# Kernel tuning notes

Hardware: AMD Instinct MI355X
Metric: run time of the kernel (lower is better)

The kernel has to match this reference:

```python
import jax, jax.numpy as jnp
import numpy as np

V, E, H, B, S, C = 50000, 300, 512, 128, 80, 6
HH = 2 * H  # hidden_dim * num_directions (BiDi=True)


def _gru_dir(x, w_ih, w_hh, b_ih, b_hh, reverse):
    # x: (b, t, e) -> (b, t, h); torch nn.GRU cell math
    Bv, T, _ = x.shape
    Hd = w_hh.shape[1]
    xg = jnp.einsum('bte,ge->btg', x, w_ih) + b_ih  # (b, t, 3h)
    if reverse:
        xg = xg[:, ::-1]
    def step(h, xt):
        gi_r, gi_z, gi_n = jnp.split(xt, 3, axis=-1)
        gh_r, gh_z, gh_n = jnp.split(h @ w_hh.T + b_hh, 3, axis=-1)
        r = jax.nn.sigmoid(gi_r + gh_r)
        z = jax.nn.sigmoid(gi_z + gh_z)
        n = jnp.tanh(gi_n + r * gh_n)
        hn = (1.0 - z) * n + z * h
        return hn, hn
    h0 = jnp.zeros((Bv, Hd), x.dtype)
    _, hs = jax.lax.scan(step, h0, jnp.swapaxes(xg, 0, 1))
    hs = jnp.swapaxes(hs, 0, 1)
    if reverse:
        hs = hs[:, ::-1]
    return hs


def _bigru(x, pf, pb):
    return jnp.concatenate([_gru_dir(x, *pf, reverse=False), _gru_dir(x, *pb, reverse=True)], axis=-1)


def _conv1d(x, w, b, d):
    y = jax.lax.conv_general_dilated(x, w, (1,), 'VALID', rhs_dilation=(d,),
                                     dimension_numbers=('NCH', 'OIH', 'NCH'))
    return y + b[None, :, None]


def _bn(x, g, b, m, v):
    # eval-mode BatchNorm1d with running stats
    return (x - m[None, :, None]) * (g[None, :, None] / jnp.sqrt(v[None, :, None] + 1e-5)) + b[None, :, None]


def setup_inputs():
    key = jax.random.key(0)
    ks = iter(jax.random.split(key, 64))
    def W(*shape):
        return jax.random.normal(next(ks), shape, jnp.float32) * 0.02
    inp = {
        'input_batch': jax.random.randint(next(ks), (B, S), 1, V),
        'choices_batch': jax.random.randint(next(ks), (B, 4, C), 1, V),
        'emb_table': W(V, E),
    }
    for p in ('sg', 'cg'):
        for d in ('f', 'b'):
            inp[p + '_wih_' + d] = W(3 * H, E)
            inp[p + '_whh_' + d] = W(3 * H, H)
            inp[p + '_bih_' + d] = W(3 * H)
            inp[p + '_bhh_' + d] = W(3 * H)
    inp['lin_w'] = W(HH, HH * C)
    inp['lin_b'] = W(HH)
    inp['attn_w'] = W(HH, HH)
    inp['attn_b'] = W(HH)
    inp['c11_w'] = W(HH, S, 3);  inp['c11_b'] = W(HH)
    inp['c13_w'] = W(HH, HH, 3); inp['c13_b'] = W(HH)
    inp['c21_w'] = W(HH, HH, 3); inp['c21_b'] = W(HH)
    inp['c23_w'] = W(HH, HH, 3); inp['c23_b'] = W(HH)
    for i in ('1', '2'):
        inp['bn' + i + '_g'] = jnp.ones((HH,), jnp.float32)
        inp['bn' + i + '_b'] = jnp.zeros((HH,), jnp.float32)
        inp['bn' + i + '_m'] = jnp.zeros((HH,), jnp.float32)
        inp['bn' + i + '_v'] = jnp.ones((HH,), jnp.float32)
    inp['gate_wp'] = W(2 * HH, HH)
    inp['gate_wc'] = W(2 * HH, 2 * HH)
    inp['gate_b'] = W(2 * HH)
    inp['out_wp'] = W(2 * HH, HH)
    inp['out_b'] = W(2 * HH)
    return inp


def reference(input_batch, choices_batch, emb_table,
              sg_wih_f, sg_whh_f, sg_bih_f, sg_bhh_f, sg_wih_b, sg_whh_b, sg_bih_b, sg_bhh_b,
              cg_wih_f, cg_whh_f, cg_bih_f, cg_bhh_f, cg_wih_b, cg_whh_b, cg_bih_b, cg_bhh_b,
              lin_w, lin_b, attn_w, attn_b,
              c11_w, c11_b, c13_w, c13_b, c21_w, c21_b, c23_w, c23_b,
              bn1_g, bn1_b, bn1_m, bn1_v, bn2_g, bn2_b, bn2_m, bn2_v,
              gate_wp, gate_wc, gate_b, out_wp, out_b):
    # --- encode passage: embedding + BiGRU (dropout is eval-mode identity) ---
    sent = _bigru(emb_table[input_batch],
                  (sg_wih_f, sg_whh_f, sg_bih_f, sg_bhh_f),
                  (sg_wih_b, sg_whh_b, sg_bih_b, sg_bhh_b))  # (B, S, 2h)
    cgf = (cg_wih_f, cg_whh_f, cg_bih_f, cg_bhh_f)
    cgb = (cg_wih_b, cg_whh_b, cg_bih_b, cg_bhh_b)

    def choice_vec(tok):  # (B, C) -> (B, 2h)
        g = _bigru(emb_table[tok], cgf, cgb)               # (B, C, 2h)
        return g.reshape(g.shape[0], -1) @ lin_w.T + lin_b

    cvs = [choice_vec(choices_batch[:, i]) for i in range(4)]

    # --- AttnReader: shared Wh/bh, per-choice softmax attention over seq ---
    Wh = jnp.einsum('bsh,hg->bsg', sent, attn_w)  # (B, S, 2h)
    bh = sent @ attn_b                            # (B, S)

    def attn_read(cv):
        a = jax.nn.softmax(jnp.einsum('bsg,bg->bs', Wh, cv) + bh, axis=1)
        return jnp.einsum('bs,bsh->bh', a, sent)  # (B, 2h)

    pars = [attn_read(cv) for cv in cvs]

    # --- IDCNN: Conv1d treats seq dim S as channels (faithful to source) ---
    x = jax.nn.relu(_bn(_conv1d(sent, c11_w, c11_b, 1), bn1_g, bn1_b, bn1_m, bn1_v))
    x = _conv1d(x, c13_w, c13_b, 3)
    x = jax.nn.relu(_bn(_conv1d(x, c21_w, c21_b, 1), bn2_g, bn2_b, bn2_m, bn2_v))
    x = _conv1d(x, c23_w, c23_b, 3)
    P = jnp.max(x, axis=2)  # AdaptiveMaxPool1d(1) + squeeze -> (B, 2h)

    Cs = [jnp.concatenate([cv, par], axis=1) for cv, par in zip(cvs, pars)]  # (B, 4h)

    # --- PointerNet (note: source bug makes out1..out4 all equal C1WP+bC1) ---
    WP = P @ gate_wp.T          # (B, 4h)
    WP_out = P @ out_wp.T       # (B, 4h)
    Cd1 = Cs[0] * jax.nn.sigmoid(WP + Cs[0] @ gate_wc.T + gate_b)
    o1 = jnp.sum(Cd1 * WP_out, axis=1, keepdims=True) + (Cd1 @ out_b)[:, None]  # (B, 1)
    return jnp.concatenate([o1, o1, o1, o1], axis=1)  # (B, 4)
```

## Files before the change

### kernel.cpp

```cpp
#include <hip/hip_runtime.h>

typedef unsigned int u32;
typedef unsigned short u16;
typedef __attribute__((ext_vector_type(4))) float f32x4;
typedef __attribute__((ext_vector_type(8))) short bf16x8;

#define DEV static __device__ __forceinline__

DEV float sigf(float x){ return 1.0f/(1.0f + expf(-x)); }

DEV u16 f2bf(float x){
  u32 u = __float_as_uint(x);
  u32 r = (u + 0x7FFFu + ((u >> 16) & 1u)) >> 16;
  return (u16)r;
}

DEV u32 encf(float f){
  u32 u = __float_as_uint(f);
  return (u & 0x80000000u) ? ~u : (u | 0x80000000u);
}
DEV float decf(u32 e){
  return (e & 0x80000000u) ? __uint_as_float(e ^ 0x80000000u) : __uint_as_float(~e);
}

DEV void gload16(const void* g, void* l){
  __builtin_amdgcn_global_load_lds((const __attribute__((address_space(1))) u32*)g,
                                   (__attribute__((address_space(3))) u32*)l, 16, 0, 0);
}

__global__ __launch_bounds__(256,2) void gemm_bf16(
    const u16* __restrict__ A, const u16* __restrict__ A2,
    const u16* __restrict__ B,
    const float* __restrict__ bias, const float* __restrict__ bias2,
    float* __restrict__ C, float* __restrict__ C2, int ldc,
    int Kp, int ksteps)
{
  __shared__ u16 lds[(128 + 128)*32];
  char* ldsc = (char*)&lds[0];
  const int Boff = 128*64;
  const int tid = threadIdx.x;
  const int l = tid & 63, w = tid >> 6;
  const int n0 = blockIdx.x * 128, m0 = blockIdx.y * 128;
  const u16* Ause = blockIdx.z ? A2 : A;
  const float* buse = blockIdx.z ? bias2 : bias;
  float* Cuse = blockIdx.z ? C2 : C;
  const int wr = w >> 1, wc = w & 1;
  const int lr = l & 15, g = l >> 4;

  f32x4 acc[4][4];
  #pragma unroll
  for (int i=0;i<4;++i)
    #pragma unroll
    for (int j=0;j<4;++j) acc[i][j] = f32x4{0.f,0.f,0.f,0.f};

  for (int ks = 0; ks < ksteps; ++ks) {
    const int i0 = ks*32;
    __syncthreads();
    #pragma unroll
    for (int r = 0; r < 2; ++r) {
      const int rr = w*2 + r;
      const int c = rr*64 + l;
      const int row = c >> 2, bpos = c & 3;
      const int ib = bpos ^ (row & 3);
      gload16(Ause + ((size_t)(m0 + row)*Kp + (i0 + ib*8)), ldsc + rr*1024);
      gload16(B    + ((size_t)(n0 + row)*Kp + (i0 + ib*8)), ldsc + Boff + rr*1024);
    }
    __syncthreads();
    bf16x8 af[4], bfr[4];
    #pragma unroll
    for (int m=0;m<4;++m){
      int o = wr*64 + m*16 + lr;
      af[m] = *(const bf16x8*)(ldsc + o*64 + ((g ^ (o&3))<<4));
    }
    #pragma unroll
    for (int n=0;n<4;++n){
      int pr = wc*64 + n*16 + lr;
      bfr[n] = *(const bf16x8*)(ldsc + Boff + pr*64 + ((g ^ (pr&3))<<4));
    }
    #pragma unroll
    for (int m=0;m<4;++m)
      #pragma unroll
      for (int n=0;n<4;++n)
        acc[m][n] = __builtin_amdgcn_mfma_f32_16x16x32_bf16(af[m], bfr[n], acc[m][n], 0,0,0);
  }

  #pragma unroll
  for (int m=0;m<4;++m){
    int mm = m0 + wr*64 + m*16 + g*4;
    f32x4 bv = *(const f32x4*)(buse + mm);
    #pragma unroll
    for (int n=0;n<4;++n){
      int p = n0 + wc*64 + n*16 + lr;
      f32x4 v;
      #pragma unroll
      for (int r2=0;r2<4;++r2) v[r2] = acc[m][n][r2] + bv[r2];
      *(f32x4*)(Cuse + (size_t)p*ldc + mm) = v;
    }
  }
}

__global__ __launch_bounds__(256,2) void gemm_bf16_sk(
    const u16* __restrict__ A, const u16* __restrict__ B,
    float* __restrict__ C, int ldc, int Kp, int kpc)
{
  __shared__ u16 lds[(128 + 128)*32];
  char* ldsc = (char*)&lds[0];
  const int Boff = 128*64;
  const int tid = threadIdx.x;
  const int l = tid & 63, w = tid >> 6;
  const int n0 = blockIdx.x * 128, m0 = blockIdx.y * 128;
  const int ks0 = blockIdx.z * kpc;
  const int wr = w >> 1, wc = w & 1;
  const int lr = l & 15, g = l >> 4;

  f32x4 acc[4][4];
  #pragma unroll
  for (int i=0;i<4;++i)
    #pragma unroll
    for (int j=0;j<4;++j) acc[i][j] = f32x4{0.f,0.f,0.f,0.f};

  for (int ks = 0; ks < kpc; ++ks) {
    const int i0 = (ks0 + ks)*32;
    __syncthreads();
    #pragma unroll
    for (int r = 0; r < 2; ++r) {
      const int rr = w*2 + r;
      const int c = rr*64 + l;
      const int row = c >> 2, bpos = c & 3;
      const int ib = bpos ^ (row & 3);
      gload16(A + ((size_t)(m0 + row)*Kp + (i0 + ib*8)), ldsc + rr*1024);
      gload16(B + ((size_t)(n0 + row)*Kp + (i0 + ib*8)), ldsc + Boff + rr*1024);
    }
    __syncthreads();
    bf16x8 af[4], bfr[4];
    #pragma unroll
    for (int m=0;m<4;++m){
      int o = wr*64 + m*16 + lr;
      af[m] = *(const bf16x8*)(ldsc + o*64 + ((g ^ (o&3))<<4));
    }
    #pragma unroll
    for (int n=0;n<4;++n){
      int pr = wc*64 + n*16 + lr;
      bfr[n] = *(const bf16x8*)(ldsc + Boff + pr*64 + ((g ^ (pr&3))<<4));
    }
    #pragma unroll
    for (int m=0;m<4;++m)
      #pragma unroll
      for (int n=0;n<4;++n)
        acc[m][n] = __builtin_amdgcn_mfma_f32_16x16x32_bf16(af[m], bfr[n], acc[m][n], 0,0,0);
  }

  #pragma unroll
  for (int m=0;m<4;++m){
    int mm = m0 + wr*64 + m*16 + g*4;
    #pragma unroll
    for (int n=0;n<4;++n){
      int p = n0 + wc*64 + n*16 + lr;
      float* dst = C + (size_t)p*ldc + mm;
      #pragma unroll
      for (int r2=0;r2<4;++r2) atomicAdd(dst + r2, acc[m][n][r2]);
    }
  }
}

__global__ void initc(float* __restrict__ C, const float* __restrict__ bias,
                      int total, int mmask)
{
  int i = blockIdx.x*256 + threadIdx.x;
  if (i < total) C[i] = bias ? bias[i & mmask] : 0.f;
}

__global__ __launch_bounds__(256) void gru_step(
    const float* __restrict__ xg0, const float* __restrict__ xg1,
    const float* __restrict__ whh0, const float* __restrict__ whh1,
    const float* __restrict__ bhh0, const float* __restrict__ bhh1,
    float* __restrict__ hs, int S, int t)
{
  __shared__ float hL[32*520];
  __shared__ float wL[48*132];
  const int tid = threadIdx.x;
  const int tj = tid & 15, tb = tid >> 4;
  const int jg = blockIdx.x;
  const int b0 = blockIdx.y*32;
  const int dir = blockIdx.z;
  const int l = tid & 63, w = tid >> 6;
  const float* xg  = dir ? xg1  : xg0;
  const float* whh = dir ? whh1 : whh0;
  const float* bhh = dir ? bhh1 : bhh0;
  const int tt = dir ? (S-1-t) : t;
  const int j = jg*16 + tj;

  float accr[2], accz[2], accn[2];
  {
    float br = bhh[j], bz = bhh[512+j], bn = bhh[1024+j];
    accr[0]=br; accr[1]=br; accz[0]=bz; accz[1]=bz; accn[0]=bn; accn[1]=bn;
  }

  if (t > 0){
    const int tp = dir ? (tt+1) : (tt-1);
    #pragma unroll
    for (int rr = 0; rr < 8; ++rr){
      int row = w*8 + rr;
      const float* srcb = hs + ((size_t)(b0+row)*S + tp)*1024 + dir*512;
      gload16(srcb + l*4,       (char*)hL + (size_t)(row*520)*4);
      gload16(srcb + 256 + l*4, (char*)hL + (size_t)(row*520 + 256)*4);
    }
    for (int c = 0; c < 4; ++c){
      const int k0 = c*128;
      __syncthreads();
      #pragma unroll
      for (int i = 0; i < 6; ++i){
        int qidx = tid + i*256;
        int row = qidx >> 5, q = qidx & 31;
        int grow = (row>>4)*512 + jg*16 + (row & 15);
        f32x4 v = *(const f32x4*)(whh + (size_t)grow*512 + k0 + q*4);
        *(f32x4*)(wL + row*132 + q*4) = v;
      }
      __syncthreads();
      #pragma unroll 4
      for (int q = 0; q < 32; ++q){
        f32x4 ha  = *(const f32x4*)(hL + (2*tb  )*520 + k0 + q*4);
        f32x4 hb  = *(const f32x4*)(hL + (2*tb+1)*520 + k0 + q*4);
        f32x4 wr4 = *(const f32x4*)(wL + tj*132      + q*4);
        f32x4 wz4 = *(const f32x4*)(wL + (16+tj)*132 + q*4);
        f32x4 wn4 = *(const f32x4*)(wL + (32+tj)*132 + q*4);
        #pragma unroll
        for (int e = 0; e < 4; ++e){
          accr[0] += ha[e]*wr4[e]; accz[0] += ha[e]*wz4[e]; accn[0] += ha[e]*wn4[e];
          accr[1] += hb[e]*wr4[e]; accz[1] += hb[e]*wz4[e]; accn[1] += hb[e]*wn4[e];
        }
      }
    }
  }

  #pragma unroll
  for (int bi = 0; bi < 2; ++bi){
    int lb = 2*tb + bi;
    int b = b0 + lb;
    size_t xbase = ((size_t)b*S + tt)*1536;
    float gir = xg[xbase + j], giz = xg[xbase + 512 + j], gin = xg[xbase + 1024 + j];
    float hp = (t>0) ? hL[lb*520 + j] : 0.f;
    float r = sigf(gir + accr[bi]);
    float z = sigf(giz + accz[bi]);
    float n = tanhf(gin + r*accn[bi]);
    hs[((size_t)b*S + tt)*1024 + dir*512 + j] = (1.f - z)*n + z*hp;
  }
}

__global__ void transpose_sent(const float* __restrict__ sent, u16* __restrict__ sentT)
{
  __shared__ float tl[80][65];
  int b = blockIdx.y, h0 = blockIdx.x*64;
  for (int idx = threadIdx.x; idx < 80*64; idx += 256){
    int s = idx >> 6, hh = idx & 63;
    tl[s][hh] = sent[((size_t)b*80 + s)*1024 + h0 + hh];
  }
  __syncthreads();
  for (int idx = threadIdx.x; idx < 64*96; idx += 256){
    int hh = idx / 96, s = idx % 96;
    sentT[((size_t)b*1024 + h0 + hh)*96 + s] = (s < 80) ? f2bf(tl[s][hh]) : (u16)0;
  }
}

__global__ void attn_scores(const float* __restrict__ sent, const float* __restrict__ u,
                            const float* __restrict__ attn_b, float* __restrict__ sc)
{
  int wid = blockIdx.x*4 + (threadIdx.x >> 6);
  int lane = threadIdx.x & 63;
  const float* row = sent + (size_t)wid*1024;
  const float* ub = u + (size_t)(wid/80)*1024;
  float acc = 0.f;
  for (int h = lane; h < 1024; h += 64) acc += row[h]*(ub[h] + attn_b[h]);
  #pragma unroll
  for (int m = 32; m; m >>= 1) acc += __shfl_xor(acc, m);
  if (lane == 0) sc[wid] = acc;
}

__global__ void softmax80(const float* __restrict__ sc, float* __restrict__ a)
{
  __shared__ float sv[80];
  __shared__ float inv;
  int b = blockIdx.x, t = threadIdx.x;
  if (t < 80) sv[t] = sc[b*80 + t];
  __syncthreads();
  if (t == 0){
    float mx = -1e30f;
    for (int s = 0; s < 80; ++s) mx = fmaxf(mx, sv[s]);
    float sum = 0.f;
    for (int s = 0; s < 80; ++s){ float e = expf(sv[s]-mx); sv[s] = e; sum += e; }
    inv = 1.f/sum;
  }
  __syncthreads();
  if (t < 80) a[b*80 + t] = sv[t]*inv;
}

__global__ void par_cs0(const float* __restrict__ a, const float* __restrict__ sent,
                        const float* __restrict__ cv, float* __restrict__ Cs0)
{
  int b = blockIdx.x;
  for (int h = threadIdx.x; h < 1024; h += 256){
    float acc = 0.f;
    for (int s = 0; s < 80; ++s) acc += a[b*80+s]*sent[((size_t)b*80+s)*1024 + h];
    Cs0[(size_t)b*2048 + 1024 + h] = acc;
    Cs0[(size_t)b*2048 + h] = cv[(size_t)b*1024 + h];
  }
}

__global__ void pack_w(const float* __restrict__ src, u16* __restrict__ dst,
                       int O, int CIs, int CIp)
{
  int i = blockIdx.x*256 + threadIdx.x;
  int total = 3*O*CIp;
  if (i >= total) return;
  int tap = i/(O*CIp); int rem = i%(O*CIp); int o = rem/CIp, ci = rem%CIp;
  float v = (ci < CIs) ? src[((size_t)o*CIs + ci)*3 + tap] : 0.f;
  dst[((size_t)tap*O + o)*CIp + ci] = f2bf(v);
}

__global__ void pack_wk(const float* __restrict__ src, u16* __restrict__ dst,
                        int M, int Ks, int Kp)
{
  int i = blockIdx.x*256 + threadIdx.x;
  if (i >= M*Kp) return;
  int row = i/Kp, k = i%Kp;
  dst[i] = (k < Ks) ? f2bf(src[(size_t)row*Ks + k]) : (u16)0;
}

__global__ void pack_f2b(const float* __restrict__ src, u16* __restrict__ dst, int n)
{
  int i = blockIdx.x*256 + threadIdx.x;
  if (i < n) dst[i] = f2bf(src[i]);
}

__global__ void pack_x(const float* __restrict__ emb, const int* __restrict__ toks,
                       int rdiv, int rmul, u16* __restrict__ dst, int R)
{
  int i = blockIdx.x*256 + threadIdx.x;
  if (i >= R*320) return;
  int row = i/320, k = i%320;
  int tok = toks[(row/rdiv)*rmul + (row%rdiv)];
  dst[i] = (k < 300) ? f2bf(emb[(size_t)tok*300 + k]) : (u16)0;
}

__global__ void prep_ab(const float* c11b, const float* c13b, const float* c21b, const float* c23b,
                        const float* g1, const float* b1, const float* m1, const float* v1,
                        const float* g2, const float* b2, const float* m2, const float* v2,
                        float* ab)
{
  int i = blockIdx.x*256 + threadIdx.x;
  if (i >= 4096) return;
  int layer = i >> 10, o = i & 1023;
  float al, be;
  if (layer == 0){ al = g1[o]/sqrtf(v1[o]+1e-5f); be = c11b[o]*al + b1[o] - m1[o]*al; }
  else if (layer == 1){ al = 1.f; be = c13b[o]; }
  else if (layer == 2){ al = g2[o]/sqrtf(v2[o]+1e-5f); be = c21b[o]*al + b2[o] - m2[o]*al; }
  else { al = 1.f; be = c23b[o]; }
  ab[layer*2048 + o] = al;
  ab[layer*2048 + 1024 + o] = be;
}

__global__ void init_penc(u32* p){
  int i = blockIdx.x*256 + threadIdx.x;
  if (i < 128*1024) p[i] = encf(-3.3e38f);
}
__global__ void dec_p(const u32* __restrict__ pe, float* __restrict__ pf){
  int i = blockIdx.x*256 + threadIdx.x;
  if (i < 128*1024) pf[i] = decf(pe[i]);
}

__global__ __launch_bounds__(512,4) void conv_mfma(
    const u16* __restrict__ X, long bstrideX,
    const u16* __restrict__ Wt,
    const float* __restrict__ alpha, const float* __restrict__ beta,
    u16* __restrict__ Y, long bstrideY,
    u32* __restrict__ Penc, int b0,
    int P_in, int P_out, int CI, int dil, int ksteps, int mode)
{
  __shared__ u16 lds[(384 + 272)*32];
  char* ldsc = (char*)&lds[0];
  const int Boff = 384*64;
  const int tid = threadIdx.x;
  const int l = tid & 63, w = tid >> 6;
  const int p0 = blockIdx.x * 256, o0 = blockIdx.y * 128;
  const int bz = blockIdx.z;
  const u16* Xb = X + (size_t)bz * (size_t)bstrideX;
  const int wr = w >> 2, wc = w & 3;
  const int lr = l & 15, g = l >> 4;

  f32x4 acc[4][4];
  #pragma unroll
  for (int i=0;i<4;++i)
    #pragma unroll
    for (int j=0;j<4;++j) acc[i][j] = f32x4{0.f,0.f,0.f,0.f};

  for (int ks = 0; ks < ksteps; ++ks) {
    const int i0 = ks*32;
    __syncthreads();
    #pragma unroll
    for (int r = 0; r < 3; ++r) {
      const int c = r*512 + tid;
      const int row = c >> 2, bpos = c & 3;
      const int tap = row >> 7, o = row & 127;
      const int ib = bpos ^ (o & 3);
      gload16(Wt + ((size_t)(tap*1024 + o0 + o)*CI + (i0 + ib*8)), ldsc + (size_t)c*16);
    }
    #pragma unroll
    for (int r = 0; r < 3; ++r) {
      const int c = r*512 + tid;
      if (c < 1088){
        const int row = c >> 2, bpos = c & 3;
        const int ib = bpos ^ (row & 3);
        int ps = p0 + row; ps = ps < P_in ? ps : (P_in - 1);
        gload16(Xb + ((size_t)ps*CI + (i0 + ib*8)), ldsc + Boff + (size_t)c*16);
      }
    }
    __syncthreads();
    #pragma unroll
    for (int tap = 0; tap < 3; ++tap) {
      bf16x8 af[4], bfr[4];
      #pragma unroll
      for (int m=0;m<4;++m){
        int o = wr*64 + m*16 + lr;
        af[m] = *(const bf16x8*)(ldsc + (tap*128 + o)*64 + ((g ^ (o&3))<<4));
      }
      #pragma unroll
      for (int n=0;n<4;++n){
        int pr = wc*64 + n*16 + lr + dil*tap;
        bfr[n] = *(const bf16x8*)(ldsc + Boff + pr*64 + ((g ^ (pr&3))<<4));
      }
      #pragma unroll
      for (int m=0;m<4;++m)
        #pragma unroll
        for (int n=0;n<4;++n)
          acc[m][n] = __builtin_amdgcn_mfma_f32_16x16x32_bf16(af[m], bfr[n], acc[m][n], 0,0,0);
    }
  }

  if (mode == 2) {
    #pragma unroll
    for (int m=0;m<4;++m){
      int oo = o0 + wr*64 + m*16 + g*4;
      f32x4 al = *(const f32x4*)(alpha + oo);
      f32x4 be = *(const f32x4*)(beta + oo);
      float vm[4] = {-1e30f,-1e30f,-1e30f,-1e30f};
      #pragma unroll
      for (int n=0;n<4;++n){
        int p = p0 + wc*64 + n*16 + lr;
        bool ok = p < P_out;
        #pragma unroll
        for (int r2=0;r2<4;++r2){
          float v = acc[m][n][r2]*al[r2] + be[r2];
          vm[r2] = ok ? fmaxf(vm[r2], v) : vm[r2];
        }
      }
      #pragma unroll
      for (int r2=0;r2<4;++r2){
        float v = vm[r2];
        #pragma unroll
        for (int mask=1; mask<16; mask<<=1) v = fmaxf(v, __shfl_xor(v, mask));
        if (lr == 0) atomicMax(&Penc[(size_t)(b0+bz)*1024 + oo + r2], encf(v));
      }
    }
  } else {
    #pragma unroll
    for (int m=0;m<4;++m){
      int oo = o0 + wr*64 + m*16 + g*4;
      f32x4 al = *(const f32x4*)(alpha + oo);
      f32x4 be = *(const f32x4*)(beta + oo);
      #pragma unroll
      for (int n=0;n<4;++n){
        int p = p0 + wc*64 + n*16 + lr;
        if (p < P_out){
          float v0 = acc[m][n][0]*al[0] + be[0];
          float v1 = acc[m][n][1]*al[1] + be[1];
          float v2 = acc[m][n][2]*al[2] + be[2];
          float v3 = acc[m][n][3]*al[3] + be[3];
          if (mode == 0){ v0=fmaxf(v0,0.f); v1=fmaxf(v1,0.f); v2=fmaxf(v2,0.f); v3=fmaxf(v3,0.f); }
          uint2 pk;
          pk.x = (u32)f2bf(v0) | ((u32)f2bf(v1) << 16);
          pk.y = (u32)f2bf(v2) | ((u32)f2bf(v3) << 16);
          *(uint2*)(Y + (size_t)bz*(size_t)bstrideY + (size_t)p*1024 + oo) = pk;
        }
      }
    }
  }
}

__global__ void head_final(const float* __restrict__ Cs0, const float* __restrict__ t1,
                           const float* __restrict__ t2, const float* __restrict__ outb,
                           float* __restrict__ dout)
{
  __shared__ float red[256];
  int b = blockIdx.x;
  float part = 0.f;
  for (int gg = threadIdx.x; gg < 2048; gg += 256){
    float cd = Cs0[(size_t)b*2048+gg] * sigf(t1[(size_t)b*2048+gg]);
    part += cd * (t2[(size_t)b*2048+gg] + outb[gg]);
  }
  red[threadIdx.x] = part;
  __syncthreads();
  for (int s = 128; s > 0; s >>= 1){
    if (threadIdx.x < s) red[threadIdx.x] += red[threadIdx.x + s];
    __syncthreads();
  }
  if (threadIdx.x < 4) dout[b*4 + threadIdx.x] = red[0];
}

extern "C" void kernel_launch(void* const* d_in, const int* in_sizes, int n_in,
                              void* d_out, int out_size, void* d_ws, size_t ws_size,
                              hipStream_t stream)
{
  (void)in_sizes; (void)n_in; (void)out_size; (void)ws_size;
  const int*   input_batch = (const int*)d_in[0];
  const int*   choices     = (const int*)d_in[1];
  const float* emb    = (const float*)d_in[2];
  const float* sgwihf = (const float*)d_in[3];
  const float* sgwhhf = (const float*)d_in[4];
  const float* sgbihf = (const float*)d_in[5];
  const float* sgbhhf = (const float*)d_in[6];
  const float* sgwihb = (const float*)d_in[7];
  const float* sgwhhb = (const float*)d_in[8];
  const float* sgbihb = (const float*)d_in[9];
  const float* sgbhhb = (const float*)d_in[10];
  const float* cgwihf = (const float*)d_in[11];
  const float* cgwhhf = (const float*)d_in[12];
  const float* cgbihf = (const float*)d_in[13];
  const float* cgbhhf = (const float*)d_in[14];
  const float* cgwihb = (const float*)d_in[15];
  const float* cgwhhb = (const float*)d_in[16];
  const float* cgbihb = (const float*)d_in[17];
  const float* cgbhhb = (const float*)d_in[18];
  const float* lin_w  = (const float*)d_in[19];
  const float* lin_b  = (const float*)d_in[20];
  const float* attn_w = (const float*)d_in[21];
  const float* attn_b = (const float*)d_in[22];
  const float* c11w = (const float*)d_in[23];
  const float* c11b = (const float*)d_in[24];
  const float* c13w = (const float*)d_in[25];
  const float* c13b = (const float*)d_in[26];
  const float* c21w = (const float*)d_in[27];
  const float* c21b = (const float*)d_in[28];
  const float* c23w = (const float*)d_in[29];
  const float* c23b = (const float*)d_in[30];
  const float* bn1g = (const float*)d_in[31];
  const float* bn1b = (const float*)d_in[32];
  const float* bn1m = (const float*)d_in[33];
  const float* bn1v = (const float*)d_in[34];
  const float* bn2g = (const float*)d_in[35];
  const float* bn2b = (const float*)d_in[36];
  const float* bn2m = (const float*)d_in[37];
  const float* bn2v = (const float*)d_in[38];
  const float* gatewp = (const float*)d_in[39];
  const float* gatewc = (const float*)d_in[40];
  const float* gateb  = (const float*)d_in[41];
  const float* outwp  = (const float*)d_in[42];
  const float* outb   = (const float*)d_in[43];
  float* dout = (float*)d_out;

  char* ws = (char*)d_ws; size_t off = 0;
  auto alc = [&](size_t n)->char*{ char* p = ws + off; off = (off + n + 255) & ~(size_t)255; return p; };
  float* xg_f  = (float*)alc((size_t)128*80*1536*4);
  float* xg_b  = (float*)alc((size_t)128*80*1536*4);
  float* xg_cf = (float*)alc((size_t)128*6*1536*4);
  float* xg_cb = (float*)alc((size_t)128*6*1536*4);
  float* gh    = (float*)alc((size_t)2*128*1536*4); (void)gh;
  float* sent  = (float*)alc((size_t)128*80*1024*4);
  float* g_c   = (float*)alc((size_t)128*6*1024*4);
  u16*   sentT = (u16*)alc((size_t)128*1024*96*2);
  float* cv    = (float*)alc((size_t)128*1024*4);
  float* uu    = (float*)alc((size_t)128*1024*4);
  float* scb   = (float*)alc((size_t)128*80*4);
  float* aw    = (float*)alc((size_t)128*80*4);
  float* Cs0   = (float*)alc((size_t)128*2048*4);
  u16* W1p = (u16*)alc((size_t)3*1024*96*2);
  u16* W2p = (u16*)alc((size_t)3*1024*1024*2);
  u16* W3p = (u16*)alc((size_t)3*1024*1024*2);
  u16* W4p = (u16*)alc((size_t)3*1024*1024*2);
  float* ab  = (float*)alc((size_t)4*2048*4);
  u32*  Penc = (u32*)alc((size_t)128*1024*4);
  float* Pf  = (float*)alc((size_t)128*1024*4);
  float* t1  = (float*)alc((size_t)128*2048*4);
  float* t2  = (float*)alc((size_t)128*2048*4);
  u16* xbf_s = (u16*)alc((size_t)10240*320*2);
  u16* xbf_c = (u16*)alc((size_t)768*320*2);
  u16* Wsf = (u16*)alc((size_t)1536*320*2);
  u16* Wsb = (u16*)alc((size_t)1536*320*2);
  u16* Wcf = (u16*)alc((size_t)1536*320*2);
  u16* Wcb = (u16*)alc((size_t)1536*320*2);

  char* R1 = (char*)xg_f;
  u16* linw_bf  = (u16*)(R1);
  u16* attnw_bf = (u16*)(R1 + 12582912);
  u16* gcbf     = (u16*)(R1 + 14680064);
  u16* cvbf     = (u16*)(R1 + 16252928);
  const int bc = 16;
  u16* Y0 = (u16*)(R1 + 16515072);
  u16* Y1 = Y0 + (size_t)bc*1024*1024;
  char* R2 = (char*)sent;
  u16* gwp_bf = (u16*)(R2);
  u16* gwc_bf = (u16*)(R2 + 4194304);
  u16* owp_bf = (u16*)(R2 + 12582912);
  u16* Pfbf   = (u16*)(R2 + 16777216);
  u16* Cs0bf  = (u16*)(R2 + 17039360);

  dim3 T(256), T5(512);

  pack_w<<<dim3((3*1024*96+255)/256), T, 0, stream>>>(c11w, W1p, 1024, 80, 96);
  pack_w<<<dim3((3*1024*1024+255)/256), T, 0, stream>>>(c13w, W2p, 1024, 1024, 1024);
  pack_w<<<dim3((3*1024*1024+255)/256), T, 0, stream>>>(c21w, W3p, 1024, 1024, 1024);
  pack_w<<<dim3((3*1024*1024+255)/256), T, 0, stream>>>(c23w, W4p, 1024, 1024, 1024);
  pack_wk<<<dim3((1536*320+255)/256), T, 0, stream>>>(sgwihf, Wsf, 1536, 300, 320);
  pack_wk<<<dim3((1536*320+255)/256), T, 0, stream>>>(sgwihb, Wsb, 1536, 300, 320);
  pack_wk<<<dim3((1536*320+255)/256), T, 0, stream>>>(cgwihf, Wcf, 1536, 300, 320);
  pack_wk<<<dim3((1536*320+255)/256), T, 0, stream>>>(cgwihb, Wcb, 1536, 300, 320);
  pack_x<<<dim3((10240*320+255)/256), T, 0, stream>>>(emb, input_batch, 80, 80, xbf_s, 10240);
  pack_x<<<dim3((768*320+255)/256), T, 0, stream>>>(emb, choices, 6, 24, xbf_c, 768);
  prep_ab<<<16, T, 0, stream>>>(c11b, c13b, c21b, c23b,
                                bn1g,bn1b,bn1m,bn1v, bn2g,bn2b,bn2m,bn2v, ab);
  init_penc<<<512, T, 0, stream>>>(Penc);

  gemm_bf16<<<dim3(80,12,2), T, 0, stream>>>(Wsf, Wsb, xbf_s, sgbihf, sgbihb,
                                             xg_f, xg_b, 1536, 320, 10);
  gemm_bf16<<<dim3(6,12,2), T, 0, stream>>>(Wcf, Wcb, xbf_c, cgbihf, cgbihb,
                                            xg_cf, xg_cb, 1536, 320, 10);

  for (int t = 0; t < 80; ++t)
    gru_step<<<dim3(32,4,2), T, 0, stream>>>(xg_f, xg_b, sgwhhf, sgwhhb,
                                             sgbhhf, sgbhhb, sent, 80, t);
  for (int t = 0; t < 6; ++t)
    gru_step<<<dim3(32,4,2), T, 0, stream>>>(xg_cf, xg_cb, cgwhhf, cgwhhb,
                                             cgbhhf, cgbhhb, g_c, 6, t);

  pack_wk<<<dim3((1024*6144+255)/256), T, 0, stream>>>(lin_w, linw_bf, 1024, 6144, 6144);
  pack_wk<<<dim3((1024*1024+255)/256), T, 0, stream>>>(attn_w, attnw_bf, 1024, 1024, 1024);
  pack_f2b<<<dim3((128*6144+255)/256), T, 0, stream>>>(g_c, gcbf, 128*6144);

  transpose_sent<<<dim3(16,128), T, 0, stream>>>(sent, sentT);

  initc<<<dim3((128*1024+255)/256), T, 0, stream>>>(cv, lin_b, 128*1024, 1023);
  gemm_bf16_sk<<<dim3(1,8,6), T, 0, stream>>>(linw_bf, gcbf, cv, 1024, 6144, 32);
  pack_f2b<<<dim3((128*1024+255)/256), T, 0, stream>>>(cv, cvbf, 128*1024);
  initc<<<dim3((128*1024+255)/256), T, 0, stream>>>(uu, nullptr, 128*1024, 1023);
  gemm_bf16_sk<<<dim3(1,8,2), T, 0, stream>>>(attnw_bf, cvbf, uu, 1024, 1024, 16);
  attn_scores<<<2560, T, 0, stream>>>(sent, uu, attn_b, scb);
  softmax80<<<128, dim3(128), 0, stream>>>(scb, aw);
  par_cs0<<<128, T, 0, stream>>>(aw, sent, cv, Cs0);

  pack_wk<<<dim3((2048*1024+255)/256), T, 0, stream>>>(gatewp, gwp_bf, 2048, 1024, 1024);
  pack_wk<<<dim3((2048*2048+255)/256), T, 0, stream>>>(gatewc, gwc_bf, 2048, 2048, 2048);
  pack_wk<<<dim3((2048*1024+255)/256), T, 0, stream>>>(outwp, owp_bf, 2048, 1024, 1024);
  pack_f2b<<<dim3((128*2048+255)/256), T, 0, stream>>>(Cs0, Cs0bf, 128*2048);

  for (int b0 = 0; b0 < 128; b0 += bc){
    conv_mfma<<<dim3(4,8,bc), T5, 0, stream>>>(sentT + (size_t)b0*1024*96, (long)1024*96,
        W1p, ab+0,    ab+1024, Y0, (long)1024*1024, nullptr, 0, 1024, 1022, 96,   1, 3,  0);
    conv_mfma<<<dim3(4,8,bc), T5, 0, stream>>>(Y0, (long)1024*1024,
        W2p, ab+2048, ab+3072, Y1, (long)1024*1024, nullptr, 0, 1022, 1016, 1024, 3, 32, 1);
    conv_mfma<<<dim3(4,8,bc), T5, 0, stream>>>(Y1, (long)1024*1024,
        W3p, ab+4096, ab+5120, Y0, (long)1024*1024, nullptr, 0, 1016, 1014, 1024, 1, 32, 0);
    conv_mfma<<<dim3(4,8,bc), T5, 0, stream>>>(Y0, (long)1024*1024,
        W4p, ab+6144, ab+7168, nullptr, 0, Penc, b0,          1014, 1008, 1024, 3, 32, 2);
  }
  dec_p<<<512, T, 0, stream>>>(Penc, Pf);
  pack_f2b<<<dim3((128*1024+255)/256), T, 0, stream>>>(Pf, Pfbf, 128*1024);

  initc<<<dim3((128*2048+255)/256), T, 0, stream>>>(t1, gateb, 128*2048, 2047);
  gemm_bf16_sk<<<dim3(1,16,2), T, 0, stream>>>(gwp_bf, Pfbf, t1, 2048, 1024, 16);
  gemm_bf16_sk<<<dim3(1,16,4), T, 0, stream>>>(gwc_bf, Cs0bf, t1, 2048, 2048, 16);
  initc<<<dim3((128*2048+255)/256), T, 0, stream>>>(t2, nullptr, 128*2048, 2047);
  gemm_bf16_sk<<<dim3(1,16,2), T, 0, stream>>>(owp_bf, Pfbf, t2, 2048, 1024, 16);
  head_final<<<128, T, 0, stream>>>(Cs0, t1, t2, outb, dout);
}
```

Before: 3.994 ms.

## Double-buffer conv MFMA with 256-row tiles, new LDS swizzle, wave softmax

The conv MFMA kernel now stages each K-step into one of two LDS buffers, so the next step's loads overlap the current step's MFMAs. Output-channel tiles grow to 256 rows per block (8 M-fragments per wave), and the grid is remapped so neighbouring workgroups share tiles, aiming for more reuse per load. The LDS XOR swizzle in the conv and GEMM kernels changes from row&3 to (row>>1)&3 to reduce bank conflicts, and softmax80 becomes a single-wave shuffle reduction. The larger LDS footprint and accumulator set lower occupancy (launch bounds drop to 2 blocks), which could hurt latency hiding.

```diff
diff --git a/kernel.cpp b/kernel.cpp
--- a/kernel.cpp
+++ b/kernel.cpp
@@ -61,7 +61,7 @@
       const int rr = w*2 + r;
       const int c = rr*64 + l;
       const int row = c >> 2, bpos = c & 3;
-      const int ib = bpos ^ (row & 3);
+      const int ib = bpos ^ ((row>>1) & 3);
       gload16(Ause + ((size_t)(m0 + row)*Kp + (i0 + ib*8)), ldsc + rr*1024);
       gload16(B    + ((size_t)(n0 + row)*Kp + (i0 + ib*8)), ldsc + Boff + rr*1024);
     }
@@ -70,12 +70,12 @@
     #pragma unroll
     for (int m=0;m<4;++m){
       int o = wr*64 + m*16 + lr;
-      af[m] = *(const bf16x8*)(ldsc + o*64 + ((g ^ (o&3))<<4));
+      af[m] = *(const bf16x8*)(ldsc + o*64 + ((g ^ ((o>>1)&3))<<4));
     }
     #pragma unroll
     for (int n=0;n<4;++n){
       int pr = wc*64 + n*16 + lr;
-      bfr[n] = *(const bf16x8*)(ldsc + Boff + pr*64 + ((g ^ (pr&3))<<4));
+      bfr[n] = *(const bf16x8*)(ldsc + Boff + pr*64 + ((g ^ ((pr>>1)&3))<<4));
     }
     #pragma unroll
     for (int m=0;m<4;++m)
@@ -127,7 +127,7 @@
       const int rr = w*2 + r;
       const int c = rr*64 + l;
       const int row = c >> 2, bpos = c & 3;
-      const int ib = bpos ^ (row & 3);
+      const int ib = bpos ^ ((row>>1) & 3);
       gload16(A + ((size_t)(m0 + row)*Kp + (i0 + ib*8)), ldsc + rr*1024);
       gload16(B + ((size_t)(n0 + row)*Kp + (i0 + ib*8)), ldsc + Boff + rr*1024);
     }
@@ -136,12 +136,12 @@
     #pragma unroll
     for (int m=0;m<4;++m){
       int o = wr*64 + m*16 + lr;
-      af[m] = *(const bf16x8*)(ldsc + o*64 + ((g ^ (o&3))<<4));
+      af[m] = *(const bf16x8*)(ldsc + o*64 + ((g ^ ((o>>1)&3))<<4));
     }
     #pragma unroll
     for (int n=0;n<4;++n){
       int pr = wc*64 + n*16 + lr;
-      bfr[n] = *(const bf16x8*)(ldsc + Boff + pr*64 + ((g ^ (pr&3))<<4));
+      bfr[n] = *(const bf16x8*)(ldsc + Boff + pr*64 + ((g ^ ((pr>>1)&3))<<4));
     }
     #pragma unroll
     for (int m=0;m<4;++m)
@@ -278,20 +278,20 @@
 
 __global__ void softmax80(const float* __restrict__ sc, float* __restrict__ a)
 {
-  __shared__ float sv[80];
-  __shared__ float inv;
-  int b = blockIdx.x, t = threadIdx.x;
-  if (t < 80) sv[t] = sc[b*80 + t];
-  __syncthreads();
-  if (t == 0){
-    float mx = -1e30f;
-    for (int s = 0; s < 80; ++s) mx = fmaxf(mx, sv[s]);
-    float sum = 0.f;
-    for (int s = 0; s < 80; ++s){ float e = expf(sv[s]-mx); sv[s] = e; sum += e; }
-    inv = 1.f/sum;
-  }
-  __syncthreads();
-  if (t < 80) a[b*80 + t] = sv[t]*inv;
+  int b = blockIdx.x, l = threadIdx.x;
+  float v0 = sc[b*80 + l];
+  float v1 = (l < 16) ? sc[b*80 + 64 + l] : -1e30f;
+  float mx = fmaxf(v0, v1);
+  #pragma unroll
+  for (int m = 32; m; m >>= 1) mx = fmaxf(mx, __shfl_xor(mx, m));
+  float e0 = expf(v0 - mx);
+  float e1 = (l < 16) ? expf(v1 - mx) : 0.f;
+  float s = e0 + e1;
+  #pragma unroll
+  for (int m = 32; m; m >>= 1) s += __shfl_xor(s, m);
+  float inv = 1.f/s;
+  a[b*80 + l] = e0*inv;
+  if (l < 16) a[b*80 + 64 + l] = e1*inv;
 }
 
 __global__ void par_cs0(const float* __restrict__ a, const float* __restrict__ sent,
@@ -368,7 +368,7 @@
   if (i < 128*1024) pf[i] = decf(pe[i]);
 }
 
-__global__ __launch_bounds__(512,4) void conv_mfma(
+__global__ __launch_bounds__(512,2) void conv_mfma(
     const u16* __restrict__ X, long bstrideX,
     const u16* __restrict__ Wt,
     const float* __restrict__ alpha, const float* __restrict__ beta,
@@ -376,32 +376,35 @@
     u32* __restrict__ Penc, int b0,
     int P_in, int P_out, int CI, int dil, int ksteps, int mode)
 {
-  __shared__ u16 lds[(384 + 272)*32];
+  __shared__ u16 lds[2*66560/2];
   char* ldsc = (char*)&lds[0];
-  const int Boff = 384*64;
+  const int BUF = 66560;
+  const int BOFF = 768*64;
   const int tid = threadIdx.x;
   const int l = tid & 63, w = tid >> 6;
-  const int p0 = blockIdx.x * 256, o0 = blockIdx.y * 128;
-  const int bz = blockIdx.z;
+  const int wg = blockIdx.x + (blockIdx.y<<2) + (blockIdx.z<<4);
+  const int id2 = ((wg & 7) << 5) | (wg >> 3);
+  const int p0 = (id2 & 3) * 256;
+  const int o0 = ((id2 >> 2) & 3) * 256;
+  const int bz = id2 >> 4;
   const u16* Xb = X + (size_t)bz * (size_t)bstrideX;
   const int wr = w >> 2, wc = w & 3;
   const int lr = l & 15, g = l >> 4;
 
-  f32x4 acc[4][4];
-  #pragma unroll
-  for (int i=0;i<4;++i)
+  f32x4 acc[8][4];
+  #pragma unroll
+  for (int i=0;i<8;++i)
     #pragma unroll
     for (int j=0;j<4;++j) acc[i][j] = f32x4{0.f,0.f,0.f,0.f};
 
-  for (int ks = 0; ks < ksteps; ++ks) {
-    const int i0 = ks*32;
-    __syncthreads();
-    #pragma unroll
-    for (int r = 0; r < 3; ++r) {
+  {
+    const int i0 = 0;
+    #pragma unroll
+    for (int r = 0; r < 6; ++r) {
       const int c = r*512 + tid;
       const int row = c >> 2, bpos = c & 3;
-      const int tap = row >> 7, o = row & 127;
-      const int ib = bpos ^ (o & 3);
+      const int tap = row >> 8, o = row & 255;
+      const int ib = bpos ^ ((row>>1) & 3);
       gload16(Wt + ((size_t)(tap*1024 + o0 + o)*CI + (i0 + ib*8)), ldsc + (size_t)c*16);
     }
     #pragma unroll
@@ -409,37 +412,64 @@
       const int c = r*512 + tid;
       if (c < 1088){
         const int row = c >> 2, bpos = c & 3;
-        const int ib = bpos ^ (row & 3);
+        const int ib = bpos ^ ((row>>1) & 3);
         int ps = p0 + row; ps = ps < P_in ? ps : (P_in - 1);
-        gload16(Xb + ((size_t)ps*CI + (i0 + ib*8)), ldsc + Boff + (size_t)c*16);
-      }
-    }
-    __syncthreads();
+        gload16(Xb + ((size_t)ps*CI + (i0 + ib*8)), ldsc + BOFF + (size_t)c*16);
+      }
+    }
+  }
+  __syncthreads();
+
+  for (int ks = 0; ks < ksteps; ++ks) {
+    const int cur = ks & 1;
+    if (ks + 1 < ksteps) {
+      const int i0 = (ks+1)*32;
+      char* dst = ldsc + (cur^1)*BUF;
+      #pragma unroll
+      for (int r = 0; r < 6; ++r) {
+        const int c = r*512 + tid;
+        const int row = c >> 2, bpos = c & 3;
+        const int tap = row >> 8, o = row & 255;
+        const int ib = bpos ^ ((row>>1) & 3);
+        gload16(Wt + ((size_t)(tap*1024 + o0 + o)*CI + (i0 + ib*8)), dst + (size_t)c*16);
+      }
+      #pragma unroll
+      for (int r = 0; r < 3; ++r) {
+        const int c = r*512 + tid;
+        if (c < 1088){
+          const int row = c >> 2, bpos = c & 3;
+          const int ib = bpos ^ ((row>>1) & 3);
+          int ps = p0 + row; ps = ps < P_in ? ps : (P_in - 1);
+          gload16(Xb + ((size_t)ps*CI + (i0 + ib*8)), dst + BOFF + (size_t)c*16);
+        }
+      }
+    }
+    char* src = ldsc + cur*BUF;
     #pragma unroll
     for (int tap = 0; tap < 3; ++tap) {
-      bf16x8 af[4], bfr[4];
-      #pragma unroll
-      for (int m=0;m<4;++m){
-        int o = wr*64 + m*16 + lr;
-        af[m] = *(const bf16x8*)(ldsc + (tap*128 + o)*64 + ((g ^ (o&3))<<4));
+      bf16x8 af[8];
+      #pragma unroll
+      for (int m=0;m<8;++m){
+        int o = wr*128 + m*16 + lr;
+        int row = tap*256 + o;
+        af[m] = *(const bf16x8*)(src + row*64 + ((g ^ ((row>>1)&3))<<4));
       }
       #pragma unroll
       for (int n=0;n<4;++n){
         int pr = wc*64 + n*16 + lr + dil*tap;
-        bfr[n] = *(const bf16x8*)(ldsc + Boff + pr*64 + ((g ^ (pr&3))<<4));
-      }
-      #pragma unroll
-      for (int m=0;m<4;++m)
+        bf16x8 bfr = *(const bf16x8*)(src + BOFF + pr*64 + ((g ^ ((pr>>1)&3))<<4));
         #pragma unroll
-        for (int n=0;n<4;++n)
-          acc[m][n] = __builtin_amdgcn_mfma_f32_16x16x32_bf16(af[m], bfr[n], acc[m][n], 0,0,0);
-    }
+        for (int m=0;m<8;++m)
+          acc[m][n] = __builtin_amdgcn_mfma_f32_16x16x32_bf16(af[m], bfr, acc[m][n], 0,0,0);
+      }
+    }
+    __syncthreads();
   }
 
   if (mode == 2) {
     #pragma unroll
-    for (int m=0;m<4;++m){
-      int oo = o0 + wr*64 + m*16 + g*4;
+    for (int m=0;m<8;++m){
+      int oo = o0 + wr*128 + m*16 + g*4;
       f32x4 al = *(const f32x4*)(alpha + oo);
       f32x4 be = *(const f32x4*)(beta + oo);
       float vm[4] = {-1e30f,-1e30f,-1e30f,-1e30f};
@@ -463,8 +493,8 @@
     }
   } else {
     #pragma unroll
-    for (int m=0;m<4;++m){
-      int oo = o0 + wr*64 + m*16 + g*4;
+    for (int m=0;m<8;++m){
+      int oo = o0 + wr*128 + m*16 + g*4;
       f32x4 al = *(const f32x4*)(alpha + oo);
       f32x4 be = *(const f32x4*)(beta + oo);
       #pragma unroll
@@ -643,7 +673,7 @@
   initc<<<dim3((128*1024+255)/256), T, 0, stream>>>(uu, nullptr, 128*1024, 1023);
   gemm_bf16_sk<<<dim3(1,8,2), T, 0, stream>>>(attnw_bf, cvbf, uu, 1024, 1024, 16);
   attn_scores<<<2560, T, 0, stream>>>(sent, uu, attn_b, scb);
-  softmax80<<<128, dim3(128), 0, stream>>>(scb, aw);
+  softmax80<<<128, dim3(64), 0, stream>>>(scb, aw);
   par_cs0<<<128, T, 0, stream>>>(aw, sent, cv, Cs0);
 
   pack_wk<<<dim3((2048*1024+255)/256), T, 0, stream>>>(gatewp, gwp_bf, 2048, 1024, 1024);
@@ -652,13 +682,13 @@
   pack_f2b<<<dim3((128*2048+255)/256), T, 0, stream>>>(Cs0, Cs0bf, 128*2048);
 
   for (int b0 = 0; b0 < 128; b0 += bc){
-    conv_mfma<<<dim3(4,8,bc), T5, 0, stream>>>(sentT + (size_t)b0*1024*96, (long)1024*96,
+    conv_mfma<<<dim3(4,4,bc), T5, 0, stream>>>(sentT + (size_t)b0*1024*96, (long)1024*96,
         W1p, ab+0,    ab+1024, Y0, (long)1024*1024, nullptr, 0, 1024, 1022, 96,   1, 3,  0);
-    conv_mfma<<<dim3(4,8,bc), T5, 0, stream>>>(Y0, (long)1024*1024,
+    conv_mfma<<<dim3(4,4,bc), T5, 0, stream>>>(Y0, (long)1024*1024,
         W2p, ab+2048, ab+3072, Y1, (long)1024*1024, nullptr, 0, 1022, 1016, 1024, 3, 32, 1);
-    conv_mfma<<<dim3(4,8,bc), T5, 0, stream>>>(Y1, (long)1024*1024,
+    conv_mfma<<<dim3(4,4,bc), T5, 0, stream>>>(Y1, (long)1024*1024,
         W3p, ab+4096, ab+5120, Y0, (long)1024*1024, nullptr, 0, 1016, 1014, 1024, 1, 32, 0);
-    conv_mfma<<<dim3(4,8,bc), T5, 0, stream>>>(Y0, (long)1024*1024,
+    conv_mfma<<<dim3(4,4,bc), T5, 0, stream>>>(Y0, (long)1024*1024,
         W4p, ab+6144, ab+7168, nullptr, 0, Penc, b0,          1014, 1008, 1024, 3, 32, 2);
   }
   dec_p<<<512, T, 0, stream>>>(Penc, Pf);
```

Measured after the change: 3.720 ms. -6.9%, faster.
